# Kernel tuning notes

Hardware: AMD Instinct MI355X
Metric: run time of the kernel (lower is better)

The kernel has to match this reference:

```python
import jax, jax.numpy as jnp
import numpy as np

# Model config (matches init_kwargs)
B, T, D = 2, 2048, 2048
H, KH, F = 16, 4, 8192
HD = D // H            # 128
G = H // KH            # q heads per kv head = 4
EPS = 1e-5


def _ln(x, g, b):
    m = jnp.mean(x, axis=-1, keepdims=True)
    v = jnp.mean((x - m) ** 2, axis=-1, keepdims=True)
    return (x - m) * jax.lax.rsqrt(v + EPS) * g + b


def setup_inputs() -> dict:
    key = jax.random.key(0)
    ks = jax.random.split(key, 8)

    def xav(k, shape):
        lim = (6.0 / (shape[0] + shape[1])) ** 0.5
        return jax.random.uniform(k, shape, jnp.float32, -lim, lim)

    x = jax.random.normal(ks[0], (B, T, D), jnp.float32)
    mask = jnp.tril(jnp.ones((1, 1, T, T), jnp.int32))  # causal
    # Linear weights stored as [in, out] (transpose of torch nn.Linear)
    return {
        "x": x,
        "mask": mask,
        "Wq": xav(ks[1], (D, H * HD)), "bq": jnp.zeros((H * HD,), jnp.float32),
        "Wk": xav(ks[2], (D, KH * HD)), "bk": jnp.zeros((KH * HD,), jnp.float32),
        "Wv": xav(ks[3], (D, KH * HD)), "bv": jnp.zeros((KH * HD,), jnp.float32),
        "Wo": xav(ks[4], (H * HD, D)), "bo": jnp.zeros((D,), jnp.float32),
        "ln1_g": jnp.ones((D,), jnp.float32), "ln1_b": jnp.zeros((D,), jnp.float32),
        "ln2_g": jnp.ones((D,), jnp.float32), "ln2_b": jnp.zeros((D,), jnp.float32),
        "fln_g": jnp.ones((D,), jnp.float32), "fln_b": jnp.zeros((D,), jnp.float32),
        "W1": xav(ks[5], (D, F)), "b1": jnp.zeros((F,), jnp.float32),
        "W2": xav(ks[6], (D, F)), "b2": jnp.zeros((F,), jnp.float32),
        "W3": xav(ks[7], (F, D)), "b3": jnp.zeros((D,), jnp.float32),
    }


def reference(x, mask, Wq, bq, Wk, bk, Wv, bv, Wo, bo,
              ln1_g, ln1_b, ln2_g, ln2_b, fln_g, fln_b,
              W1, b1, W2, b2, W3, b3):
    scale = 1.0 / np.sqrt(HD)
    # --- attention block (pre-LN + residual) ---
    h = _ln(x, ln1_g, ln1_b)
    q = (h @ Wq + bq).reshape(B, T, KH, G, HD)   # q head k*G+g uses kv head k
    k = (h @ Wk + bk).reshape(B, T, KH, HD)
    v = (h @ Wv + bv).reshape(B, T, KH, HD)
    # GQA scores without repeat_interleave: broadcast kv head across group g
    scores = jnp.einsum('btkgd,bskd->bkgts', q, k) * scale  # [B,KH,G,T,T]
    scores = jnp.clip(scores, -100.0, 100.0)
    scores = jnp.where(mask[:, :, None] == 0, -jnp.inf, scores)
    attn = jax.nn.softmax(scores, axis=-1)
    ctx = jnp.einsum('bkgts,bskd->btkgd', attn, v).reshape(B, T, H * HD)
    x = x + (ctx @ Wo + bo)  # dropout is identity in eval
    # --- ln2 then SwiGLU FFN (which has its own internal LN and residual
    # around the *post-ln2* activation, faithful to original) ---
    x = _ln(x, ln2_g, ln2_b)
    r = x
    h2 = _ln(x, fln_g, fln_b)
    g_pre = h2 @ W1 + b1
    gate = g_pre * jax.nn.sigmoid(jnp.clip(g_pre, -10.0, 10.0))
    hidden = h2 @ W2 + b2
    return r + ((gate * hidden) @ W3 + b3)
```

## Files before the change

kernel.cpp:

```cpp
#include <hip/hip_runtime.h>
#include <math.h>
#include <stdint.h>

typedef __bf16 bf16_t;
typedef __bf16 bf16x4 __attribute__((ext_vector_type(4)));
typedef __bf16 bf16x8 __attribute__((ext_vector_type(8)));
typedef float  f32x4  __attribute__((ext_vector_type(4)));

#define D_MODEL 2048
#define T_SEQ   2048
#define BATCH   2
#define NROWS   (BATCH*T_SEQ)
#define NHEAD   16
#define HDIM    128
#define KVH     4
#define KVD     (KVH*HDIM)
#define FDIM    8192
#define QKVN    3072

__device__ __forceinline__ bf16x8 mk8(bf16x4 lo, bf16x4 hi) {
  union { bf16x4 h[2]; bf16x8 v; } u;
  u.h[0] = lo; u.h[1] = hi; return u.v;
}

__device__ __forceinline__ void gl16(const bf16_t* g, bf16_t* l) {
  __builtin_amdgcn_global_load_lds(
      (const uint32_t __attribute__((address_space(1)))*)g,
      (uint32_t __attribute__((address_space(3)))*)l, 16, 0, 0);
}

__global__ __launch_bounds__(256)
void transpose_w(const float* __restrict__ in, bf16_t* __restrict__ outT, int K, int N)
{
  __shared__ __align__(16) bf16_t t[64][72];
  const int tid = threadIdx.x;
  const int k0 = blockIdx.y * 64, n0 = blockIdx.x * 64;
  const int tr = tid >> 4, tc = (tid & 15) * 4;
#pragma unroll
  for (int i = 0; i < 4; ++i) {
    f32x4 v = *(const f32x4*)(in + (size_t)(k0 + tr + 16 * i) * N + n0 + tc);
#pragma unroll
    for (int e = 0; e < 4; ++e) t[tr + 16 * i][tc + e] = (bf16_t)v[e];
  }
  __syncthreads();
#pragma unroll
  for (int s = 0; s < 2; ++s) {
    const int c = s * 256 + tid;
    const int n = c >> 3, c8 = (c & 7) * 8;
    bf16x8 o;
#pragma unroll
    for (int e = 0; e < 8; ++e) o[e] = t[c8 + e][n];
    *(bf16x8*)(outT + (size_t)(n0 + n) * K + k0 + c8) = o;
  }
}

__global__ __launch_bounds__(256)
void concat_bias(const float* __restrict__ a, const float* __restrict__ b,
                 const float* __restrict__ c, float* __restrict__ dst)
{
  const int i = blockIdx.x * 256 + threadIdx.x;
  if (i >= QKVN) return;
  dst[i] = (i < 2048) ? a[i] : (i < 2560) ? b[i - 2048] : c[i - 2560];
}

template<typename TI>
__global__ __launch_bounds__(256)
void ln_kernel(const TI* __restrict__ x, const float* __restrict__ g,
               const float* __restrict__ b, bf16_t* __restrict__ out)
{
  const int row = blockIdx.x;
  const int tid = threadIdx.x;
  const TI* xr = x + (size_t)row * D_MODEL;
  float vals[8];
  if constexpr (sizeof(TI) == 4) {
    f32x4 v0 = *(const f32x4*)(xr + tid * 8);
    f32x4 v1 = *(const f32x4*)(xr + tid * 8 + 4);
#pragma unroll
    for (int e = 0; e < 4; ++e) { vals[e] = v0[e]; vals[4 + e] = v1[e]; }
  } else {
    bf16x8 v = *(const bf16x8*)(xr + tid * 8);
#pragma unroll
    for (int e = 0; e < 8; ++e) vals[e] = (float)v[e];
  }
  float s = 0.f, s2 = 0.f;
#pragma unroll
  for (int e = 0; e < 8; ++e) { s += vals[e]; s2 += vals[e] * vals[e]; }
#pragma unroll
  for (int off = 1; off < 64; off <<= 1) { s += __shfl_xor(s, off); s2 += __shfl_xor(s2, off); }
  __shared__ float red[8];
  const int wid = tid >> 6, lane = tid & 63;
  if (lane == 0) { red[wid] = s; red[4 + wid] = s2; }
  __syncthreads();
  s  = red[0] + red[1] + red[2] + red[3];
  s2 = red[4] + red[5] + red[6] + red[7];
  const float mean = s * (1.f / D_MODEL);
  const float var  = s2 * (1.f / D_MODEL) - mean * mean;
  const float rstd = rsqrtf(var + 1e-5f);
  f32x4 g0 = *(const f32x4*)(g + tid * 8), g1 = *(const f32x4*)(g + tid * 8 + 4);
  f32x4 b0 = *(const f32x4*)(b + tid * 8), b1 = *(const f32x4*)(b + tid * 8 + 4);
  bf16x8 o;
#pragma unroll
  for (int e = 0; e < 4; ++e) {
    o[e]     = (bf16_t)((vals[e]     - mean) * rstd * g0[e] + b0[e]);
    o[4 + e] = (bf16_t)((vals[4 + e] - mean) * rstd * g1[e] + b1[e]);
  }
  *(bf16x8*)(out + (size_t)row * D_MODEL + tid * 8) = o;
}

__global__ __launch_bounds__(256)
void ln2_fused(const bf16_t* __restrict__ x, const float* __restrict__ g2,
               const float* __restrict__ b2, const float* __restrict__ gf,
               const float* __restrict__ bf_, bf16_t* __restrict__ rout,
               bf16_t* __restrict__ hout)
{
  const int row = blockIdx.x;
  const int tid = threadIdx.x;
  const int wid = tid >> 6, lane = tid & 63;
  __shared__ float red[8];
  const bf16_t* xr = x + (size_t)row * D_MODEL;
  bf16x8 v = *(const bf16x8*)(xr + tid * 8);
  float vals[8]; float s = 0.f, s2 = 0.f;
#pragma unroll
  for (int e = 0; e < 8; ++e) { vals[e] = (float)v[e]; s += vals[e]; s2 += vals[e] * vals[e]; }
#pragma unroll
  for (int off = 1; off < 64; off <<= 1) { s += __shfl_xor(s, off); s2 += __shfl_xor(s2, off); }
  if (lane == 0) { red[wid] = s; red[4 + wid] = s2; }
  __syncthreads();
  s  = red[0] + red[1] + red[2] + red[3];
  s2 = red[4] + red[5] + red[6] + red[7];
  float mean = s * (1.f / D_MODEL);
  float var  = s2 * (1.f / D_MODEL) - mean * mean;
  float rstd = rsqrtf(var + 1e-5f);
  f32x4 ga0 = *(const f32x4*)(g2 + tid * 8), ga1 = *(const f32x4*)(g2 + tid * 8 + 4);
  f32x4 ba0 = *(const f32x4*)(b2 + tid * 8), ba1 = *(const f32x4*)(b2 + tid * 8 + 4);
  float y[8];
#pragma unroll
  for (int e = 0; e < 4; ++e) {
    y[e]     = (vals[e]     - mean) * rstd * ga0[e] + ba0[e];
    y[4 + e] = (vals[4 + e] - mean) * rstd * ga1[e] + ba1[e];
  }
  bf16x8 o1;
#pragma unroll
  for (int e = 0; e < 8; ++e) o1[e] = (bf16_t)y[e];
  *(bf16x8*)(rout + (size_t)row * D_MODEL + tid * 8) = o1;
  s = 0.f; s2 = 0.f;
#pragma unroll
  for (int e = 0; e < 8; ++e) { s += y[e]; s2 += y[e] * y[e]; }
#pragma unroll
  for (int off = 1; off < 64; off <<= 1) { s += __shfl_xor(s, off); s2 += __shfl_xor(s2, off); }
  __syncthreads();
  if (lane == 0) { red[wid] = s; red[4 + wid] = s2; }
  __syncthreads();
  s  = red[0] + red[1] + red[2] + red[3];
  s2 = red[4] + red[5] + red[6] + red[7];
  mean = s * (1.f / D_MODEL);
  var  = s2 * (1.f / D_MODEL) - mean * mean;
  rstd = rsqrtf(var + 1e-5f);
  f32x4 gb0 = *(const f32x4*)(gf + tid * 8), gb1 = *(const f32x4*)(gf + tid * 8 + 4);
  f32x4 bb0 = *(const f32x4*)(bf_ + tid * 8), bb1 = *(const f32x4*)(bf_ + tid * 8 + 4);
  bf16x8 o2;
#pragma unroll
  for (int e = 0; e < 4; ++e) {
    o2[e]     = (bf16_t)((y[e]     - mean) * rstd * gb0[e] + bb0[e]);
    o2[4 + e] = (bf16_t)((y[4 + e] - mean) * rstd * gb1[e] + bb1[e]);
  }
  *(bf16x8*)(hout + (size_t)row * D_MODEL + tid * 8) = o2;
}

enum { EPI_NONE = 0, EPI_RES = 1, EPI_SILU = 2, EPI_MUL = 3 };

__device__ __forceinline__ void xcd_swz(int BMv, int BNv, int& m0, int& n0) {
  const int nbx = gridDim.x, nwg = nbx * gridDim.y;
  int flat = blockIdx.y * nbx + blockIdx.x;
  flat = (flat & 7) * (nwg >> 3) + (flat >> 3);
  m0 = (flat / nbx) * BMv; n0 = (flat % nbx) * BNv;
}

template<int EPI, int BM_T, typename TE, typename TO>
__global__ __launch_bounds__(512, 2)
void gemm8p(const bf16_t* __restrict__ A, const bf16_t* __restrict__ Bt,
            const float* __restrict__ bias, const TE* __restrict__ extra,
            TO* __restrict__ out, int M, int N, int K)
{
  constexpr int ALs = BM_T / 128;
  constexpr int RF  = BM_T / 32;
  __shared__ __align__(16) bf16_t As[2][2][BM_T * 32];
  __shared__ __align__(16) bf16_t Bs[2][2][256 * 32];
  const int tid = threadIdx.x, lane = tid & 63, wid = tid >> 6;
  const int wr = wid >> 2, wc = wid & 3;
  const int l16 = lane & 15, lq = lane >> 4;
  int m0, n0; xcd_swz(BM_T, 256, m0, n0);

  const bf16_t* aP[ALs]; int aL[ALs];
#pragma unroll
  for (int s = 0; s < ALs; ++s) {
    const int c = s * 512 + tid;
    const int row = c >> 2, pos = c & 3;
    aP[s] = A + (size_t)(m0 + row) * K + (pos ^ ((row >> 1) & 3)) * 8;
    aL[s] = (s * 512 + wid * 64) * 8;
  }
  const bf16_t* bP[2]; int bL[2];
#pragma unroll
  for (int s = 0; s < 2; ++s) {
    const int c = s * 512 + tid;
    const int row = c >> 2, pos = c & 3;
    bP[s] = Bt + (size_t)(n0 + row) * K + (pos ^ ((row >> 1) & 3)) * 8;
    bL[s] = (s * 512 + wid * 64) * 8;
  }

  int offA[RF];
#pragma unroll
  for (int i = 0; i < RF; ++i) {
    const int r = wr * (BM_T / 2) + i * 16 + l16;
    offA[i] = r * 32 + ((lq ^ ((r >> 1) & 3)) * 8);
  }
  int offB[4];
#pragma unroll
  for (int jj = 0; jj < 4; ++jj) {
    const int r = wc * 64 + jj * 16 + l16;
    offB[jj] = r * 32 + ((lq ^ ((r >> 1) & 3)) * 8);
  }

  f32x4 acc[RF][4];
#pragma unroll
  for (int i = 0; i < RF; ++i)
#pragma unroll
    for (int j = 0; j < 4; ++j) acc[i][j] = (f32x4){0.f, 0.f, 0.f, 0.f};

  auto SA = [&](int t, int bb, int kh) {
#pragma unroll
    for (int s = 0; s < ALs; ++s) gl16(aP[s] + t * 64 + kh * 32, &As[bb][kh][aL[s]]);
  };
  auto SB = [&](int t, int bb, int kh) {
#pragma unroll
    for (int s = 0; s < 2; ++s) gl16(bP[s] + t * 64 + kh * 32, &Bs[bb][kh][bL[s]]);
  };
#define BAR_()  __builtin_amdgcn_s_barrier()
#define LGKM_() do { asm volatile("s_waitcnt lgkmcnt(0)" ::: "memory"); \
                     __builtin_amdgcn_sched_barrier(0); } while (0)

  const int nt = K >> 6;
  SA(0, 0, 0); SB(0, 0, 0); SA(0, 0, 1); SB(0, 0, 1);
  if (nt > 1) { SA(1, 1, 0); SB(1, 1, 0); SA(1, 1, 1); }
  if (nt > 2) {
    if constexpr (ALs == 2) asm volatile("s_waitcnt vmcnt(6)" ::: "memory");
    else                    asm volatile("s_waitcnt vmcnt(4)" ::: "memory");
  } else {
    asm volatile("s_waitcnt vmcnt(0)" ::: "memory");
  }
  BAR_();

  for (int t = 0; t < nt; ++t) {
    const int b = t & 1, ob = b ^ 1;
    const bool s1 = (t + 1 < nt), s2 = (t + 2 < nt);
    bf16x8 af[RF], bf0, bf1;
    if (s1) SB(t + 1, ob, 1);
#pragma unroll
    for (int i = 0; i < RF; ++i) af[i] = *(const bf16x8*)(&As[b][0][offA[i]]);
    bf0 = *(const bf16x8*)(&Bs[b][0][offB[0]]);
    bf1 = *(const bf16x8*)(&Bs[b][0][offB[1]]);
    BAR_(); LGKM_();
    __builtin_amdgcn_s_setprio(1);
#pragma unroll
    for (int i = 0; i < RF; ++i) {
      acc[i][0] = __builtin_amdgcn_mfma_f32_16x16x32_bf16(af[i], bf0, acc[i][0], 0, 0, 0);
      acc[i][1] = __builtin_amdgcn_mfma_f32_16x16x32_bf16(af[i], bf1, acc[i][1], 0, 0, 0);
    }
    __builtin_amdgcn_s_setprio(0);
    BAR_();
    if (s2) SA(t + 2, b, 0);
    bf0 = *(const bf16x8*)(&Bs[b][0][offB[2]]);
    bf1 = *(const bf16x8*)(&Bs[b][0][offB[3]]);
    BAR_(); LGKM_();
    __builtin_amdgcn_s_setprio(1);
#pragma unroll
    for (int i = 0; i < RF; ++i) {
      acc[i][2] = __builtin_amdgcn_mfma_f32_16x16x32_bf16(af[i], bf0, acc[i][2], 0, 0, 0);
      acc[i][3] = __builtin_amdgcn_mfma_f32_16x16x32_bf16(af[i], bf1, acc[i][3], 0, 0, 0);
    }
    __builtin_amdgcn_s_setprio(0);
    BAR_();
    if (s2) SB(t + 2, b, 0);
#pragma unroll
    for (int i = 0; i < RF; ++i) af[i] = *(const bf16x8*)(&As[b][1][offA[i]]);
    bf0 = *(const bf16x8*)(&Bs[b][1][offB[0]]);
    bf1 = *(const bf16x8*)(&Bs[b][1][offB[1]]);
    BAR_(); LGKM_();
    __builtin_amdgcn_s_setprio(1);
#pragma unroll
    for (int i = 0; i < RF; ++i) {
      acc[i][0] = __builtin_amdgcn_mfma_f32_16x16x32_bf16(af[i], bf0, acc[i][0], 0, 0, 0);
      acc[i][1] = __builtin_amdgcn_mfma_f32_16x16x32_bf16(af[i], bf1, acc[i][1], 0, 0, 0);
    }
    __builtin_amdgcn_s_setprio(0);
    BAR_();
    if (s2) SA(t + 2, b, 1);
    bf0 = *(const bf16x8*)(&Bs[b][1][offB[2]]);
    bf1 = *(const bf16x8*)(&Bs[b][1][offB[3]]);
    BAR_(); LGKM_();
    __builtin_amdgcn_s_setprio(1);
#pragma unroll
    for (int i = 0; i < RF; ++i) {
      acc[i][2] = __builtin_amdgcn_mfma_f32_16x16x32_bf16(af[i], bf0, acc[i][2], 0, 0, 0);
      acc[i][3] = __builtin_amdgcn_mfma_f32_16x16x32_bf16(af[i], bf1, acc[i][3], 0, 0, 0);
    }
    __builtin_amdgcn_s_setprio(0);
    if (t < nt - 2) {
      if constexpr (ALs == 2) asm volatile("s_waitcnt vmcnt(6)" ::: "memory");
      else                    asm volatile("s_waitcnt vmcnt(4)" ::: "memory");
    } else {
      asm volatile("s_waitcnt vmcnt(0)" ::: "memory");
    }
    BAR_();
  }

  if constexpr (sizeof(TO) == 2) {
    bf16_t* sc = &As[0][0][0] + (size_t)wid * (16 * 72);
    const int rr = lane >> 3, cc8 = (lane & 7) * 8;
#pragma unroll
    for (int i = 0; i < RF; ++i) {
      const int row0 = m0 + wr * (BM_T / 2) + i * 16;
#pragma unroll
      for (int j = 0; j < 4; ++j) {
        const int col = n0 + wc * 64 + j * 16 + l16;
        const float bb = bias[col];
#pragma unroll
        for (int e = 0; e < 4; ++e) {
          const size_t idx = (size_t)(row0 + lq * 4 + e) * N + col;
          float vv = acc[i][j][e] + bb;
          if (EPI == EPI_RES)       vv += (float)extra[idx];
          else if (EPI == EPI_SILU) { float c2 = fminf(fmaxf(vv, -10.f), 10.f); vv = vv / (1.f + __expf(-c2)); }
          else if (EPI == EPI_MUL)  vv *= (float)extra[idx];
          sc[(lq * 4 + e) * 72 + j * 16 + l16] = (bf16_t)vv;
        }
      }
      asm volatile("s_waitcnt lgkmcnt(0)" ::: "memory");
      __builtin_amdgcn_sched_barrier(0);
#pragma unroll
      for (int q = 0; q < 2; ++q) {
        bf16x8 v8 = *(const bf16x8*)(sc + (rr + q * 8) * 72 + cc8);
        *(bf16x8*)(out + (size_t)(row0 + rr + q * 8) * N + n0 + wc * 64 + cc8) = v8;
      }
      asm volatile("s_waitcnt lgkmcnt(0)" ::: "memory");
      __builtin_amdgcn_sched_barrier(0);
    }
  } else {
#pragma unroll
    for (int j = 0; j < 4; ++j) {
      const int col = n0 + wc * 64 + j * 16 + l16;
      const float bb = bias[col];
#pragma unroll
      for (int i = 0; i < RF; ++i) {
        const int row0 = m0 + wr * (BM_T / 2) + i * 16 + lq * 4;
#pragma unroll
        for (int e = 0; e < 4; ++e) {
          const size_t idx = (size_t)(row0 + e) * N + col;
          float vv = acc[i][j][e] + bb;
          if (EPI == EPI_RES)       vv += (float)extra[idx];
          else if (EPI == EPI_SILU) { float c2 = fminf(fmaxf(vv, -10.f), 10.f); vv = vv / (1.f + __expf(-c2)); }
          else if (EPI == EPI_MUL)  vv *= (float)extra[idx];
          out[idx] = (TO)vv;
        }
      }
    }
  }
#undef BAR_
#undef LGKM_
}

template<int EPI, typename TE, typename TO>
__global__ __launch_bounds__(512, 2)
void gemm2p(const bf16_t* __restrict__ A, const bf16_t* __restrict__ Bt,
            const float* __restrict__ bias, const TE* __restrict__ extra,
            TO* __restrict__ out, int M, int N, int K)
{
  __shared__ __align__(16) bf16_t As[2][2][128 * 32];
  __shared__ __align__(16) bf16_t Bs[2][2][256 * 32];
  const int tid = threadIdx.x, lane = tid & 63, wid = tid >> 6;
  const int wr = wid >> 2, wc = wid & 3;
  const int l16 = lane & 15, lq = lane >> 4;
  int m0, n0; xcd_swz(128, 256, m0, n0);

  const bf16_t* aP; int aL;
  {
    const int row = tid >> 2, pos = tid & 3;
    aP = A + (size_t)(m0 + row) * K + (pos ^ ((row >> 1) & 3)) * 8;
    aL = (wid * 64) * 8;
  }
  const bf16_t* bP[2]; int bL[2];
#pragma unroll
  for (int s = 0; s < 2; ++s) {
    const int c = s * 512 + tid;
    const int row = c >> 2, pos = c & 3;
    bP[s] = Bt + (size_t)(n0 + row) * K + (pos ^ ((row >> 1) & 3)) * 8;
    bL[s] = (s * 512 + wid * 64) * 8;
  }

  int offA[4], offB[4];
#pragma unroll
  for (int i = 0; i < 4; ++i) {
    const int r = wr * 64 + i * 16 + l16;
    offA[i] = r * 32 + ((lq ^ ((r >> 1) & 3)) * 8);
  }
#pragma unroll
  for (int j = 0; j < 4; ++j) {
    const int r = wc * 64 + j * 16 + l16;
    offB[j] = r * 32 + ((lq ^ ((r >> 1) & 3)) * 8);
  }

  f32x4 acc[4][4];
#pragma unroll
  for (int i = 0; i < 4; ++i)
#pragma unroll
    for (int j = 0; j < 4; ++j) acc[i][j] = (f32x4){0.f, 0.f, 0.f, 0.f};

  auto SA = [&](int t, int bb, int kh) { gl16(aP + t * 64 + kh * 32, &As[bb][kh][aL]); };
  auto SB = [&](int t, int bb, int kh) {
#pragma unroll
    for (int s = 0; s < 2; ++s) gl16(bP[s] + t * 64 + kh * 32, &Bs[bb][kh][bL[s]]);
  };

  const int nt = K >> 6;
  SA(0, 0, 0); SB(0, 0, 0); SA(0, 0, 1); SB(0, 0, 1);
  if (nt > 1) {
    SA(1, 1, 0); SB(1, 1, 0);
    asm volatile("s_waitcnt vmcnt(3)" ::: "memory");
  } else {
    asm volatile("s_waitcnt vmcnt(0)" ::: "memory");
  }
  __builtin_amdgcn_s_barrier();

  for (int t = 0; t < nt; ++t) {
    const int b = t & 1, ob = b ^ 1;
    bf16x8 af[4], bfr[4];
    if (t + 1 < nt) { SA(t + 1, ob, 1); SB(t + 1, ob, 1); }
#pragma unroll
    for (int i = 0; i < 4; ++i) af[i]  = *(const bf16x8*)(&As[b][0][offA[i]]);
#pragma unroll
    for (int j = 0; j < 4; ++j) bfr[j] = *(const bf16x8*)(&Bs[b][0][offB[j]]);
    __builtin_amdgcn_s_barrier();
    asm volatile("s_waitcnt lgkmcnt(0)" ::: "memory");
    __builtin_amdgcn_sched_barrier(0);
    __builtin_amdgcn_s_setprio(1);
#pragma unroll
    for (int i = 0; i < 4; ++i)
#pragma unroll
      for (int j = 0; j < 4; ++j)
        acc[i][j] = __builtin_amdgcn_mfma_f32_16x16x32_bf16(af[i], bfr[j], acc[i][j], 0, 0, 0);
    __builtin_amdgcn_s_setprio(0);
    __builtin_amdgcn_s_barrier();
    if (t + 2 < nt) { SA(t + 2, b, 0); SB(t + 2, b, 0); }
#pragma unroll
    for (int i = 0; i < 4; ++i) af[i]  = *(const bf16x8*)(&As[b][1][offA[i]]);
#pragma unroll
    for (int j = 0; j < 4; ++j) bfr[j] = *(const bf16x8*)(&Bs[b][1][offB[j]]);
    if (t + 2 < nt) asm volatile("s_waitcnt vmcnt(3)" ::: "memory");
    else            asm volatile("s_waitcnt vmcnt(0)" ::: "memory");
    __builtin_amdgcn_s_barrier();
    asm volatile("s_waitcnt lgkmcnt(0)" ::: "memory");
    __builtin_amdgcn_sched_barrier(0);
    __builtin_amdgcn_s_setprio(1);
#pragma unroll
    for (int i = 0; i < 4; ++i)
#pragma unroll
      for (int j = 0; j < 4; ++j)
        acc[i][j] = __builtin_amdgcn_mfma_f32_16x16x32_bf16(af[i], bfr[j], acc[i][j], 0, 0, 0);
    __builtin_amdgcn_s_setprio(0);
    __builtin_amdgcn_s_barrier();
  }

  if constexpr (sizeof(TO) == 2) {
    bf16_t* sc = &As[0][0][0] + (size_t)wid * (16 * 72);
    const int rr = lane >> 3, cc8 = (lane & 7) * 8;
#pragma unroll
    for (int i = 0; i < 4; ++i) {
      const int row0 = m0 + wr * 64 + i * 16;
#pragma unroll
      for (int j = 0; j < 4; ++j) {
        const int col = n0 + wc * 64 + j * 16 + l16;
        const float bb = bias[col];
#pragma unroll
        for (int e = 0; e < 4; ++e) {
          const size_t idx = (size_t)(row0 + lq * 4 + e) * N + col;
          float vv = acc[i][j][e] + bb;
          if (EPI == EPI_RES)       vv += (float)extra[idx];
          else if (EPI == EPI_SILU) { float c2 = fminf(fmaxf(vv, -10.f), 10.f); vv = vv / (1.f + __expf(-c2)); }
          else if (EPI == EPI_MUL)  vv *= (float)extra[idx];
          sc[(lq * 4 + e) * 72 + j * 16 + l16] = (bf16_t)vv;
        }
      }
      asm volatile("s_waitcnt lgkmcnt(0)" ::: "memory");
      __builtin_amdgcn_sched_barrier(0);
#pragma unroll
      for (int q = 0; q < 2; ++q) {
        bf16x8 v8 = *(const bf16x8*)(sc + (rr + q * 8) * 72 + cc8);
        *(bf16x8*)(out + (size_t)(row0 + rr + q * 8) * N + n0 + wc * 64 + cc8) = v8;
      }
      asm volatile("s_waitcnt lgkmcnt(0)" ::: "memory");
      __builtin_amdgcn_sched_barrier(0);
    }
  } else {
#pragma unroll
    for (int j = 0; j < 4; ++j) {
      const int col = n0 + wc * 64 + j * 16 + l16;
      const float bb = bias[col];
#pragma unroll
      for (int i = 0; i < 4; ++i) {
        const int row0 = m0 + wr * 64 + i * 16 + lq * 4;
#pragma unroll
        for (int e = 0; e < 4; ++e) {
          const size_t idx = (size_t)(row0 + e) * N + col;
          float vv = acc[i][j][e] + bb;
          if (EPI == EPI_RES)       vv += (float)extra[idx];
          else if (EPI == EPI_SILU) { float c2 = fminf(fmaxf(vv, -10.f), 10.f); vv = vv / (1.f + __expf(-c2)); }
          else if (EPI == EPI_MUL)  vv *= (float)extra[idx];
          out[idx] = (TO)vv;
        }
      }
    }
  }
}

template<int EPI, typename TE, typename TO>
__global__ __launch_bounds__(256)
void gemm_kernel(const bf16_t* __restrict__ A, const float* __restrict__ W,
                 const float* __restrict__ bias, const TE* __restrict__ extra,
                 TO* __restrict__ out, int M, int N, int K)
{
  __shared__ bf16_t As[128][40];
  __shared__ bf16_t Bs[128][40];
  const int tid  = threadIdx.x;
  const int lane = tid & 63, wid = tid >> 6;
  const int wr = wid >> 1, wc = wid & 1;
  const int l16 = lane & 15, lq = lane >> 4;
  const int m0 = blockIdx.y * 128, n0 = blockIdx.x * 128;

  f32x4 acc[4][4];
#pragma unroll
  for (int i = 0; i < 4; ++i)
#pragma unroll
    for (int j = 0; j < 4; ++j) acc[i][j] = (f32x4){0.f, 0.f, 0.f, 0.f};

  const int ar = tid >> 1, ah = tid & 1;
  const int kk = tid & 31, cc = tid >> 5;

  for (int k0 = 0; k0 < K; k0 += 32) {
    const bf16_t* asrc = A + (size_t)(m0 + ar) * K + k0 + ah * 16;
    *(bf16x8*)(&As[ar][ah * 16])     = *(const bf16x8*)(asrc);
    *(bf16x8*)(&As[ar][ah * 16 + 8]) = *(const bf16x8*)(asrc + 8);
    const float* wsrc = W + (size_t)(k0 + kk) * N + n0;
#pragma unroll
    for (int it = 0; it < 2; ++it) {
      const int c = cc * 8 + it * 64;
      f32x4 wa = *(const f32x4*)(wsrc + c);
      f32x4 wb = *(const f32x4*)(wsrc + c + 4);
#pragma unroll
      for (int e = 0; e < 4; ++e) {
        Bs[c + e][kk]     = (bf16_t)wa[e];
        Bs[c + 4 + e][kk] = (bf16_t)wb[e];
      }
    }
    __syncthreads();
    bf16x8 af[4], bfr[4];
#pragma unroll
    for (int i = 0; i < 4; ++i) {
      const bf16_t* p = &As[wr * 64 + i * 16 + l16][lq * 4];
      af[i] = mk8(*(const bf16x4*)p, *(const bf16x4*)(p + 16));
    }
#pragma unroll
    for (int j = 0; j < 4; ++j) {
      const bf16_t* p = &Bs[wc * 64 + j * 16 + l16][lq * 4];
      bfr[j] = mk8(*(const bf16x4*)p, *(const bf16x4*)(p + 16));
    }
#pragma unroll
    for (int i = 0; i < 4; ++i)
#pragma unroll
      for (int j = 0; j < 4; ++j)
        acc[i][j] = __builtin_amdgcn_mfma_f32_16x16x32_bf16(af[i], bfr[j], acc[i][j], 0, 0, 0);
    __syncthreads();
  }

#pragma unroll
  for (int j = 0; j < 4; ++j) {
    const int col = n0 + wc * 64 + j * 16 + l16;
    const float bb = bias[col];
#pragma unroll
    for (int i = 0; i < 4; ++i) {
      const int row0 = m0 + wr * 64 + i * 16 + lq * 4;
#pragma unroll
      for (int e = 0; e < 4; ++e) {
        const size_t idx = (size_t)(row0 + e) * N + col;
        float vv = acc[i][j][e] + bb;
        if (EPI == EPI_RES)       vv += (float)extra[idx];
        else if (EPI == EPI_SILU) { float c2 = fminf(fmaxf(vv, -10.f), 10.f); vv = vv / (1.f + __expf(-c2)); }
        else if (EPI == EPI_MUL)  vv *= (float)extra[idx];
        out[idx] = (TO)vv;
      }
    }
  }
}

__global__ __launch_bounds__(256)
void attn_kernel(const bf16_t* __restrict__ q, const bf16_t* __restrict__ k,
                 const bf16_t* __restrict__ v, bf16_t* __restrict__ ctx,
                 int q_ld, int kv_ld)
{
  __shared__ __align__(16) bf16_t Ks[64 * 128];
  __shared__ __align__(16) bf16_t Vt[128][72];

  const int tid = threadIdx.x, lane = tid & 63, wid = tid >> 6;
  const int l16 = lane & 15, lq = lane >> 4;
  const int bh = blockIdx.y;
  const int b = bh >> 4, h = bh & 15;
  const int kh = h >> 2;
  const float scale = 0.08838834764831845f;

  for (int pass = 0; pass < 2; ++pass) {
    const int qt = pass ? blockIdx.x : (31 - blockIdx.x);
    const int qbase = qt * 64;
    const int qrow = qbase + wid * 16 + l16;

    const bf16_t* qp = q + (size_t)(b * T_SEQ + qrow) * q_ld + h * HDIM;
    bf16x8 bq[4];
#pragma unroll
    for (int s = 0; s < 4; ++s) bq[s] = *(const bf16x8*)(qp + s * 32 + lq * 8);

    float m_r = -1e30f, l_r = 0.f;
    f32x4 acc_o[8];
#pragma unroll
    for (int jh = 0; jh < 8; ++jh) acc_o[jh] = (f32x4){0.f, 0.f, 0.f, 0.f};

    const int ntiles = qt + 1;
    for (int t = 0; t < ntiles; ++t) {
      const int kb = t * 64;
      __syncthreads();
#pragma unroll
      for (int it = 0; it < 4; ++it) {
        const int c = it * 256 + tid;
        const int kvr = c >> 4, pos = c & 15;
        const int src = pos ^ (kvr & 7);
        gl16(k + (size_t)(b * T_SEQ + kb + kvr) * kv_ld + kh * HDIM + src * 8,
             Ks + (size_t)(it * 256 + wid * 64) * 8);
      }
#pragma unroll
      for (int it = 0; it < 4; ++it) {
        const int c = tid + it * 256;
        const int r = c & 63, voff = (c >> 6) * 8;
        bf16x8 vv = *(const bf16x8*)(v + (size_t)(b * T_SEQ + kb + r) * kv_ld + kh * HDIM + voff);
#pragma unroll
        for (int e = 0; e < 8; ++e) Vt[voff + e][r] = vv[e];
      }
      __syncthreads();

      f32x4 sf[4];
#pragma unroll
      for (int j = 0; j < 4; ++j) {
        sf[j] = (f32x4){0.f, 0.f, 0.f, 0.f};
        const int kvr = j * 16 + l16;
#pragma unroll
        for (int s = 0; s < 4; ++s) {
          bf16x8 ak = *(const bf16x8*)(Ks + kvr * 128 + (((s * 4 + lq) ^ (kvr & 7)) * 8));
          sf[j] = __builtin_amdgcn_mfma_f32_16x16x32_bf16(ak, bq[s], sf[j], 0, 0, 0);
        }
      }

      float p[4][4];
      float tmax = -1e30f;
#pragma unroll
      for (int j = 0; j < 4; ++j)
#pragma unroll
        for (int e = 0; e < 4; ++e) {
          const int kvc = kb + j * 16 + lq * 4 + e;
          float sv = sf[j][e] * scale;
          sv = fminf(fmaxf(sv, -100.f), 100.f);
          if (kvc > qrow) sv = -1e30f;
          p[j][e] = sv;
          tmax = fmaxf(tmax, sv);
        }
      tmax = fmaxf(tmax, __shfl_xor(tmax, 16));
      tmax = fmaxf(tmax, __shfl_xor(tmax, 32));
      const float mnew = fmaxf(m_r, tmax);
      const float resc = __expf(m_r - mnew);
      m_r = mnew;
      float rsum = 0.f;
#pragma unroll
      for (int j = 0; j < 4; ++j)
#pragma unroll
        for (int e = 0; e < 4; ++e) {
          p[j][e] = __expf(p[j][e] - m_r);
          rsum += p[j][e];
        }
      rsum += __shfl_xor(rsum, 16);
      rsum += __shfl_xor(rsum, 32);
      l_r = l_r * resc + rsum;

      float resc4[4];
#pragma unroll
      for (int e = 0; e < 4; ++e) resc4[e] = __shfl(resc, lq * 4 + e);
#pragma unroll
      for (int jh = 0; jh < 8; ++jh)
#pragma unroll
        for (int e = 0; e < 4; ++e) acc_o[jh][e] *= resc4[e];

      bf16x8 pa[2];
#pragma unroll
      for (int sk = 0; sk < 2; ++sk) {
        bf16x4 lo, hi;
#pragma unroll
        for (int e = 0; e < 4; ++e) { lo[e] = (bf16_t)p[2 * sk][e]; hi[e] = (bf16_t)p[2 * sk + 1][e]; }
        pa[sk] = mk8(lo, hi);
      }
#pragma unroll
      for (int jh = 0; jh < 8; ++jh) {
#pragma unroll
        for (int sk = 0; sk < 2; ++sk) {
          const bf16_t* pV = &Vt[jh * 16 + l16][sk * 32 + lq * 4];
          bf16x8 bv2 = mk8(*(const bf16x4*)pV, *(const bf16x4*)(pV + 16));
          acc_o[jh] = __builtin_amdgcn_mfma_f32_16x16x32_bf16(pa[sk], bv2, acc_o[jh], 0, 0, 0);
        }
      }
    }

    float l4[4];
#pragma unroll
    for (int e = 0; e < 4; ++e) l4[e] = __shfl(l_r, lq * 4 + e);
    bf16_t* op = ctx + (size_t)(b * T_SEQ + qbase + wid * 16) * D_MODEL + h * HDIM;
#pragma unroll
    for (int jh = 0; jh < 8; ++jh)
#pragma unroll
      for (int e = 0; e < 4; ++e)
        op[(size_t)(lq * 4 + e) * D_MODEL + jh * 16 + l16] = (bf16_t)(acc_o[jh][e] / l4[e]);
  }
}

extern "C" void kernel_launch(void* const* d_in, const int* in_sizes, int n_in,
                              void* d_out, int out_size, void* d_ws, size_t ws_size,
                              hipStream_t stream)
{
  const float* x   = (const float*)d_in[0];
  const float* Wq  = (const float*)d_in[2];
  const float* bq  = (const float*)d_in[3];
  const float* Wk  = (const float*)d_in[4];
  const float* bk  = (const float*)d_in[5];
  const float* Wv  = (const float*)d_in[6];
  const float* bv  = (const float*)d_in[7];
  const float* Wo  = (const float*)d_in[8];
  const float* bo  = (const float*)d_in[9];
  const float* g1  = (const float*)d_in[10];
  const float* b1n = (const float*)d_in[11];
  const float* g2  = (const float*)d_in[12];
  const float* b2n = (const float*)d_in[13];
  const float* gf  = (const float*)d_in[14];
  const float* bfn = (const float*)d_in[15];
  const float* W1  = (const float*)d_in[16];
  const float* bb1 = (const float*)d_in[17];
  const float* W2  = (const float*)d_in[18];
  const float* bb2 = (const float*)d_in[19];
  const float* W3  = (const float*)d_in[20];
  const float* bb3 = (const float*)d_in[21];
  float* out = (float*)d_out;

  char* ws = (char*)d_ws;
  size_t off = 0;
  auto alloc = [&](size_t bytes) -> void* {
    void* p = ws + off; off += (bytes + 255) & ~(size_t)255; return p;
  };
  const dim3 blk(256);

  bf16_t* Wt_qkv = (bf16_t*)alloc((size_t)QKVN * D_MODEL * 2);
  bf16_t* Wt_o   = (bf16_t*)alloc((size_t)D_MODEL * D_MODEL * 2);
  bf16_t* Wt1    = (bf16_t*)alloc((size_t)FDIM * D_MODEL * 2);
  bf16_t* Wt2    = (bf16_t*)alloc((size_t)FDIM * D_MODEL * 2);
  bf16_t* Wt3    = (bf16_t*)alloc((size_t)D_MODEL * FDIM * 2);
  float*  bqkv   = (float*)alloc((size_t)QKVN * 4);
  bf16_t* hbuf   = (bf16_t*)alloc((size_t)NROWS * D_MODEL * 2);
  bf16_t* qkvbuf = (bf16_t*)alloc((size_t)NROWS * QKVN * 2);
  bf16_t* rbuf   = (bf16_t*)alloc((size_t)NROWS * D_MODEL * 2);
  bf16_t* h2buf  = (bf16_t*)alloc((size_t)NROWS * D_MODEL * 2);
  const size_t core = off;

  if (core <= ws_size) {
    size_t avail = ws_size - core;
    int chunk = (int)((avail / ((size_t)FDIM * 2)) & ~(size_t)255);
    bf16_t* gbuf;
    if (chunk >= 256) { gbuf = (bf16_t*)(ws + core); if (chunk > NROWS) chunk = NROWS; }
    else              { gbuf = qkvbuf; chunk = 1536; }
    bf16_t* x1buf = qkvbuf;

    transpose_w<<<dim3(32, 32),  blk, 0, stream>>>(Wq, Wt_qkv, D_MODEL, 2048);
    transpose_w<<<dim3(8, 32),   blk, 0, stream>>>(Wk, Wt_qkv + (size_t)2048 * D_MODEL, D_MODEL, 512);
    transpose_w<<<dim3(8, 32),   blk, 0, stream>>>(Wv, Wt_qkv + (size_t)2560 * D_MODEL, D_MODEL, 512);
    transpose_w<<<dim3(32, 32),  blk, 0, stream>>>(Wo, Wt_o, D_MODEL, D_MODEL);
    transpose_w<<<dim3(128, 32), blk, 0, stream>>>(W1, Wt1, D_MODEL, FDIM);
    transpose_w<<<dim3(128, 32), blk, 0, stream>>>(W2, Wt2, D_MODEL, FDIM);
    transpose_w<<<dim3(32, 128), blk, 0, stream>>>(W3, Wt3, FDIM, D_MODEL);
    concat_bias<<<12, blk, 0, stream>>>(bq, bk, bv, bqkv);

    ln_kernel<float><<<NROWS, blk, 0, stream>>>(x, g1, b1n, hbuf);
    gemm8p<EPI_NONE, 256, bf16_t, bf16_t><<<dim3(QKVN / 256, NROWS / 256), 512, 0, stream>>>(
        hbuf, Wt_qkv, bqkv, nullptr, qkvbuf, NROWS, QKVN, D_MODEL);
    attn_kernel<<<dim3(16, 32), blk, 0, stream>>>(
        qkvbuf, qkvbuf + 2048, qkvbuf + 2560, hbuf, QKVN, QKVN);
    gemm2p<EPI_RES, float, bf16_t><<<dim3(D_MODEL / 256, NROWS / 128), 512, 0, stream>>>(
        hbuf, Wt_o, bo, x, x1buf, NROWS, D_MODEL, D_MODEL);
    ln2_fused<<<NROWS, blk, 0, stream>>>(x1buf, g2, b2n, gf, bfn, rbuf, h2buf);

    for (int r0 = 0; r0 < NROWS; r0 += chunk) {
      const int rows = (NROWS - r0 < chunk) ? (NROWS - r0) : chunk;
      gemm8p<EPI_SILU, 256, bf16_t, bf16_t><<<dim3(FDIM / 256, rows / 256), 512, 0, stream>>>(
          h2buf + (size_t)r0 * D_MODEL, Wt1, bb1, nullptr, gbuf, rows, FDIM, D_MODEL);
      gemm8p<EPI_MUL, 256, bf16_t, bf16_t><<<dim3(FDIM / 256, rows / 256), 512, 0, stream>>>(
          h2buf + (size_t)r0 * D_MODEL, Wt2, bb2, gbuf, gbuf, rows, FDIM, D_MODEL);
      gemm2p<EPI_RES, bf16_t, float><<<dim3(D_MODEL / 256, rows / 128), 512, 0, stream>>>(
          gbuf, Wt3, bb3, rbuf + (size_t)r0 * D_MODEL, out + (size_t)r0 * D_MODEL, rows, D_MODEL, FDIM);
    }
    return;
  }

  off = 0;
  const size_t DBYTES = (size_t)NROWS * D_MODEL * 2;
  bf16_t* fhbuf  = (bf16_t*)alloc(DBYTES);
  bf16_t* fqbuf  = (bf16_t*)alloc(DBYTES);
  bf16_t* fkbuf  = (bf16_t*)alloc((size_t)NROWS * KVD * 2);
  bf16_t* fvbuf  = (bf16_t*)alloc((size_t)NROWS * KVD * 2);
  bf16_t* frbuf  = (bf16_t*)alloc(DBYTES);
  bf16_t* fh2buf = (bf16_t*)alloc(DBYTES);
  const size_t base = off;
  size_t avail = (ws_size > base) ? (ws_size - base) : 0;
  int chunk = (int)((avail / ((size_t)FDIM * 2)) & ~(size_t)127);
  bf16_t* gbuf;
  if (chunk >= 128) { gbuf = (bf16_t*)(ws + base); if (chunk > NROWS) chunk = NROWS; }
  else              { gbuf = fqbuf; chunk = 1024; }

  ln_kernel<float><<<NROWS, blk, 0, stream>>>(x, g1, b1n, fhbuf);
  gemm_kernel<EPI_NONE, bf16_t, bf16_t><<<dim3(16, 32), blk, 0, stream>>>(fhbuf, Wq, bq, nullptr, fqbuf, NROWS, 2048, 2048);
  gemm_kernel<EPI_NONE, bf16_t, bf16_t><<<dim3(4, 32),  blk, 0, stream>>>(fhbuf, Wk, bk, nullptr, fkbuf, NROWS, 512, 2048);
  gemm_kernel<EPI_NONE, bf16_t, bf16_t><<<dim3(4, 32),  blk, 0, stream>>>(fhbuf, Wv, bv, nullptr, fvbuf, NROWS, 512, 2048);
  attn_kernel<<<dim3(16, 32), blk, 0, stream>>>(fqbuf, fkbuf, fvbuf, fhbuf, 2048, 512);
  gemm_kernel<EPI_RES, float, bf16_t><<<dim3(16, 32), blk, 0, stream>>>(fhbuf, Wo, bo, x, fqbuf, NROWS, 2048, 2048);
  ln_kernel<bf16_t><<<NROWS, blk, 0, stream>>>(fqbuf, g2, b2n, frbuf);
  ln_kernel<bf16_t><<<NROWS, blk, 0, stream>>>(frbuf, gf, bfn, fh2buf);
  for (int r0 = 0; r0 < NROWS; r0 += chunk) {
    const int rows = (NROWS - r0 < chunk) ? (NROWS - r0) : chunk;
    gemm_kernel<EPI_SILU, bf16_t, bf16_t><<<dim3(64, rows / 128), blk, 0, stream>>>(
        fh2buf + (size_t)r0 * D_MODEL, W1, bb1, nullptr, gbuf, rows, FDIM, 2048);
    gemm_kernel<EPI_MUL, bf16_t, bf16_t><<<dim3(64, rows / 128), blk, 0, stream>>>(
        fh2buf + (size_t)r0 * D_MODEL, W2, bb2, gbuf, gbuf, rows, FDIM, 2048);
    gemm_kernel<EPI_RES, bf16_t, float><<<dim3(16, rows / 128), blk, 0, stream>>>(
        gbuf, W3, bb3, frbuf + (size_t)r0 * D_MODEL, out + (size_t)r0 * D_MODEL, rows, 2048, FDIM);
  }
}
```

Baseline: 906.3 us.

## Replace 128x256 two-phase GEMM with 128x128 triple-buffered GEMM for N=2048 projections

Adds a new 256-thread GEMM kernel with 128x128 tiles, K-step 32 and a three-stage LDS ring buffer, and uses it for the output projection and the W3 down-projection in place of the 512-thread 128x256 kernel. The smaller tiles double the number of workgroups for the N=2048 GEMMs, so the GPU's compute units should be better filled and the tail wave shrinks, at the cost of lower per-block operand reuse. The 8-wave GEMM also reorders its global-to-LDS prefetch issue to come after the LDS fragment reads in each phase. That reordering changes when loads are queued relative to the LDS reads.

```diff
diff --git a/kernel.cpp b/kernel.cpp
--- a/kernel.cpp
+++ b/kernel.cpp
@@ -174,6 +174,141 @@
   int flat = blockIdx.y * nbx + blockIdx.x;
   flat = (flat & 7) * (nwg >> 3) + (flat >> 3);
   m0 = (flat / nbx) * BMv; n0 = (flat % nbx) * BNv;
+}
+
+template<int EPI, typename TE, typename TO>
+__global__ __launch_bounds__(256, 4)
+void gemm3b(const bf16_t* __restrict__ A, const bf16_t* __restrict__ Bt,
+            const float* __restrict__ bias, const TE* __restrict__ extra,
+            TO* __restrict__ out, int M, int N, int K)
+{
+  __shared__ __align__(16) bf16_t As[3][128 * 32];
+  __shared__ __align__(16) bf16_t Bs[3][128 * 32];
+  const int tid = threadIdx.x, lane = tid & 63, wid = tid >> 6;
+  const int wr = wid >> 1, wc = wid & 1;
+  const int l16 = lane & 15, lq = lane >> 4;
+  int m0, n0; xcd_swz(128, 128, m0, n0);
+
+  const bf16_t* aP[2]; const bf16_t* bP[2]; int sL[2];
+#pragma unroll
+  for (int s = 0; s < 2; ++s) {
+    const int c = s * 256 + tid;
+    const int row = c >> 2, pos = c & 3;
+    const int g = pos ^ ((row >> 1) & 3);
+    aP[s] = A  + (size_t)(m0 + row) * K + g * 8;
+    bP[s] = Bt + (size_t)(n0 + row) * K + g * 8;
+    sL[s] = (s * 256 + wid * 64) * 8;
+  }
+
+  int offA[4], offB[4];
+#pragma unroll
+  for (int i = 0; i < 4; ++i) {
+    const int r = wr * 64 + i * 16 + l16;
+    offA[i] = r * 32 + ((lq ^ ((r >> 1) & 3)) * 8);
+  }
+#pragma unroll
+  for (int j = 0; j < 4; ++j) {
+    const int r = wc * 64 + j * 16 + l16;
+    offB[j] = r * 32 + ((lq ^ ((r >> 1) & 3)) * 8);
+  }
+
+  f32x4 acc[4][4];
+#pragma unroll
+  for (int i = 0; i < 4; ++i)
+#pragma unroll
+    for (int j = 0; j < 4; ++j) acc[i][j] = (f32x4){0.f, 0.f, 0.f, 0.f};
+
+  auto STAGE = [&](int t, int b) {
+    gl16(aP[0] + t * 32, &As[b][sL[0]]);
+    gl16(aP[1] + t * 32, &As[b][sL[1]]);
+    gl16(bP[0] + t * 32, &Bs[b][sL[0]]);
+    gl16(bP[1] + t * 32, &Bs[b][sL[1]]);
+  };
+
+  const int nt = K >> 5;
+  STAGE(0, 0);
+  STAGE(1, 1);
+  if (nt > 1) asm volatile("s_waitcnt vmcnt(4)" ::: "memory");
+  else        asm volatile("s_waitcnt vmcnt(0)" ::: "memory");
+  __builtin_amdgcn_s_barrier();
+
+  int b = 0;
+  for (int t = 0; t < nt; ++t) {
+    bf16x8 af[4], bfr[4];
+#pragma unroll
+    for (int i = 0; i < 4; ++i) af[i]  = *(const bf16x8*)(&As[b][offA[i]]);
+#pragma unroll
+    for (int j = 0; j < 4; ++j) bfr[j] = *(const bf16x8*)(&Bs[b][offB[j]]);
+    if (t + 2 < nt) {
+      STAGE(t + 2, (b + 2) % 3);
+      asm volatile("s_waitcnt vmcnt(4)" ::: "memory");
+    } else {
+      asm volatile("s_waitcnt vmcnt(0)" ::: "memory");
+    }
+    __builtin_amdgcn_s_barrier();
+    asm volatile("s_waitcnt lgkmcnt(0)" ::: "memory");
+    __builtin_amdgcn_sched_barrier(0);
+    __builtin_amdgcn_s_setprio(1);
+#pragma unroll
+    for (int i = 0; i < 4; ++i)
+#pragma unroll
+      for (int j = 0; j < 4; ++j)
+        acc[i][j] = __builtin_amdgcn_mfma_f32_16x16x32_bf16(af[i], bfr[j], acc[i][j], 0, 0, 0);
+    __builtin_amdgcn_s_setprio(0);
+    __builtin_amdgcn_s_barrier();
+    b = (b + 1) % 3;
+  }
+
+  if constexpr (sizeof(TO) == 2) {
+    bf16_t* sc = &As[0][0] + (size_t)wid * (16 * 72);
+    const int rr = lane >> 3, cc8 = (lane & 7) * 8;
+#pragma unroll
+    for (int i = 0; i < 4; ++i) {
+      const int row0 = m0 + wr * 64 + i * 16;
+#pragma unroll
+      for (int j = 0; j < 4; ++j) {
+        const int col = n0 + wc * 64 + j * 16 + l16;
+        const float bb = bias[col];
+#pragma unroll
+        for (int e = 0; e < 4; ++e) {
+          const size_t idx = (size_t)(row0 + lq * 4 + e) * N + col;
+          float vv = acc[i][j][e] + bb;
+          if (EPI == EPI_RES)       vv += (float)extra[idx];
+          else if (EPI == EPI_SILU) { float c2 = fminf(fmaxf(vv, -10.f), 10.f); vv = vv / (1.f + __expf(-c2)); }
+          else if (EPI == EPI_MUL)  vv *= (float)extra[idx];
+          sc[(lq * 4 + e) * 72 + j * 16 + l16] = (bf16_t)vv;
+        }
+      }
+      asm volatile("s_waitcnt lgkmcnt(0)" ::: "memory");
+      __builtin_amdgcn_sched_barrier(0);
+#pragma unroll
+      for (int q = 0; q < 2; ++q) {
+        bf16x8 v8 = *(const bf16x8*)(sc + (rr + q * 8) * 72 + cc8);
+        *(bf16x8*)(out + (size_t)(row0 + rr + q * 8) * N + n0 + wc * 64 + cc8) = v8;
+      }
+      asm volatile("s_waitcnt lgkmcnt(0)" ::: "memory");
+      __builtin_amdgcn_sched_barrier(0);
+    }
+  } else {
+#pragma unroll
+    for (int j = 0; j < 4; ++j) {
+      const int col = n0 + wc * 64 + j * 16 + l16;
+      const float bb = bias[col];
+#pragma unroll
+      for (int i = 0; i < 4; ++i) {
+        const int row0 = m0 + wr * 64 + i * 16 + lq * 4;
+#pragma unroll
+        for (int e = 0; e < 4; ++e) {
+          const size_t idx = (size_t)(row0 + e) * N + col;
+          float vv = acc[i][j][e] + bb;
+          if (EPI == EPI_RES)       vv += (float)extra[idx];
+          else if (EPI == EPI_SILU) { float c2 = fminf(fmaxf(vv, -10.f), 10.f); vv = vv / (1.f + __expf(-c2)); }
+          else if (EPI == EPI_MUL)  vv *= (float)extra[idx];
+          out[idx] = (TO)vv;
+        }
+      }
+    }
+  }
 }
 
 template<int EPI, int BM_T, typename TE, typename TO>
@@ -254,11 +389,11 @@
     const int b = t & 1, ob = b ^ 1;
     const bool s1 = (t + 1 < nt), s2 = (t + 2 < nt);
     bf16x8 af[RF], bf0, bf1;
-    if (s1) SB(t + 1, ob, 1);
 #pragma unroll
     for (int i = 0; i < RF; ++i) af[i] = *(const bf16x8*)(&As[b][0][offA[i]]);
     bf0 = *(const bf16x8*)(&Bs[b][0][offB[0]]);
     bf1 = *(const bf16x8*)(&Bs[b][0][offB[1]]);
+    if (s1) SB(t + 1, ob, 1);
     BAR_(); LGKM_();
     __builtin_amdgcn_s_setprio(1);
 #pragma unroll
@@ -268,9 +403,9 @@
     }
     __builtin_amdgcn_s_setprio(0);
     BAR_();
-    if (s2) SA(t + 2, b, 0);
     bf0 = *(const bf16x8*)(&Bs[b][0][offB[2]]);
     bf1 = *(const bf16x8*)(&Bs[b][0][offB[3]]);
+    if (s2) SA(t + 2, b, 0);
     BAR_(); LGKM_();
     __builtin_amdgcn_s_setprio(1);
 #pragma unroll
@@ -280,11 +415,11 @@
     }
     __builtin_amdgcn_s_setprio(0);
     BAR_();
-    if (s2) SB(t + 2, b, 0);
 #pragma unroll
     for (int i = 0; i < RF; ++i) af[i] = *(const bf16x8*)(&As[b][1][offA[i]]);
     bf0 = *(const bf16x8*)(&Bs[b][1][offB[0]]);
     bf1 = *(const bf16x8*)(&Bs[b][1][offB[1]]);
+    if (s2) SB(t + 2, b, 0);
     BAR_(); LGKM_();
     __builtin_amdgcn_s_setprio(1);
 #pragma unroll
@@ -294,9 +429,9 @@
     }
     __builtin_amdgcn_s_setprio(0);
     BAR_();
-    if (s2) SA(t + 2, b, 1);
     bf0 = *(const bf16x8*)(&Bs[b][1][offB[2]]);
     bf1 = *(const bf16x8*)(&Bs[b][1][offB[3]]);
+    if (s2) SA(t + 2, b, 1);
     BAR_(); LGKM_();
     __builtin_amdgcn_s_setprio(1);
 #pragma unroll
@@ -366,159 +501,6 @@
   }
 #undef BAR_
 #undef LGKM_
-}
-
-template<int EPI, typename TE, typename TO>
-__global__ __launch_bounds__(512, 2)
-void gemm2p(const bf16_t* __restrict__ A, const bf16_t* __restrict__ Bt,
-            const float* __restrict__ bias, const TE* __restrict__ extra,
-            TO* __restrict__ out, int M, int N, int K)
-{
-  __shared__ __align__(16) bf16_t As[2][2][128 * 32];
-  __shared__ __align__(16) bf16_t Bs[2][2][256 * 32];
-  const int tid = threadIdx.x, lane = tid & 63, wid = tid >> 6;
-  const int wr = wid >> 2, wc = wid & 3;
-  const int l16 = lane & 15, lq = lane >> 4;
-  int m0, n0; xcd_swz(128, 256, m0, n0);
-
-  const bf16_t* aP; int aL;
-  {
-    const int row = tid >> 2, pos = tid & 3;
-    aP = A + (size_t)(m0 + row) * K + (pos ^ ((row >> 1) & 3)) * 8;
-    aL = (wid * 64) * 8;
-  }
-  const bf16_t* bP[2]; int bL[2];
-#pragma unroll
-  for (int s = 0; s < 2; ++s) {
-    const int c = s * 512 + tid;
-    const int row = c >> 2, pos = c & 3;
-    bP[s] = Bt + (size_t)(n0 + row) * K + (pos ^ ((row >> 1) & 3)) * 8;
-    bL[s] = (s * 512 + wid * 64) * 8;
-  }
-
-  int offA[4], offB[4];
-#pragma unroll
-  for (int i = 0; i < 4; ++i) {
-    const int r = wr * 64 + i * 16 + l16;
-    offA[i] = r * 32 + ((lq ^ ((r >> 1) & 3)) * 8);
-  }
-#pragma unroll
-  for (int j = 0; j < 4; ++j) {
-    const int r = wc * 64 + j * 16 + l16;
-    offB[j] = r * 32 + ((lq ^ ((r >> 1) & 3)) * 8);
-  }
-
-  f32x4 acc[4][4];
-#pragma unroll
-  for (int i = 0; i < 4; ++i)
-#pragma unroll
-    for (int j = 0; j < 4; ++j) acc[i][j] = (f32x4){0.f, 0.f, 0.f, 0.f};
-
-  auto SA = [&](int t, int bb, int kh) { gl16(aP + t * 64 + kh * 32, &As[bb][kh][aL]); };
-  auto SB = [&](int t, int bb, int kh) {
-#pragma unroll
-    for (int s = 0; s < 2; ++s) gl16(bP[s] + t * 64 + kh * 32, &Bs[bb][kh][bL[s]]);
-  };
-
-  const int nt = K >> 6;
-  SA(0, 0, 0); SB(0, 0, 0); SA(0, 0, 1); SB(0, 0, 1);
-  if (nt > 1) {
-    SA(1, 1, 0); SB(1, 1, 0);
-    asm volatile("s_waitcnt vmcnt(3)" ::: "memory");
-  } else {
-    asm volatile("s_waitcnt vmcnt(0)" ::: "memory");
-  }
-  __builtin_amdgcn_s_barrier();
-
-  for (int t = 0; t < nt; ++t) {
-    const int b = t & 1, ob = b ^ 1;
-    bf16x8 af[4], bfr[4];
-    if (t + 1 < nt) { SA(t + 1, ob, 1); SB(t + 1, ob, 1); }
-#pragma unroll
-    for (int i = 0; i < 4; ++i) af[i]  = *(const bf16x8*)(&As[b][0][offA[i]]);
-#pragma unroll
-    for (int j = 0; j < 4; ++j) bfr[j] = *(const bf16x8*)(&Bs[b][0][offB[j]]);
-    __builtin_amdgcn_s_barrier();
-    asm volatile("s_waitcnt lgkmcnt(0)" ::: "memory");
-    __builtin_amdgcn_sched_barrier(0);
-    __builtin_amdgcn_s_setprio(1);
-#pragma unroll
-    for (int i = 0; i < 4; ++i)
-#pragma unroll
-      for (int j = 0; j < 4; ++j)
-        acc[i][j] = __builtin_amdgcn_mfma_f32_16x16x32_bf16(af[i], bfr[j], acc[i][j], 0, 0, 0);
-    __builtin_amdgcn_s_setprio(0);
-    __builtin_amdgcn_s_barrier();
-    if (t + 2 < nt) { SA(t + 2, b, 0); SB(t + 2, b, 0); }
-#pragma unroll
-    for (int i = 0; i < 4; ++i) af[i]  = *(const bf16x8*)(&As[b][1][offA[i]]);
-#pragma unroll
-    for (int j = 0; j < 4; ++j) bfr[j] = *(const bf16x8*)(&Bs[b][1][offB[j]]);
-    if (t + 2 < nt) asm volatile("s_waitcnt vmcnt(3)" ::: "memory");
-    else            asm volatile("s_waitcnt vmcnt(0)" ::: "memory");
-    __builtin_amdgcn_s_barrier();
-    asm volatile("s_waitcnt lgkmcnt(0)" ::: "memory");
-    __builtin_amdgcn_sched_barrier(0);
-    __builtin_amdgcn_s_setprio(1);
-#pragma unroll
-    for (int i = 0; i < 4; ++i)
-#pragma unroll
-      for (int j = 0; j < 4; ++j)
-        acc[i][j] = __builtin_amdgcn_mfma_f32_16x16x32_bf16(af[i], bfr[j], acc[i][j], 0, 0, 0);
-    __builtin_amdgcn_s_setprio(0);
-    __builtin_amdgcn_s_barrier();
-  }
-
-  if constexpr (sizeof(TO) == 2) {
-    bf16_t* sc = &As[0][0][0] + (size_t)wid * (16 * 72);
-    const int rr = lane >> 3, cc8 = (lane & 7) * 8;
-#pragma unroll
-    for (int i = 0; i < 4; ++i) {
-      const int row0 = m0 + wr * 64 + i * 16;
-#pragma unroll
-      for (int j = 0; j < 4; ++j) {
-        const int col = n0 + wc * 64 + j * 16 + l16;
-        const float bb = bias[col];
-#pragma unroll
-        for (int e = 0; e < 4; ++e) {
-          const size_t idx = (size_t)(row0 + lq * 4 + e) * N + col;
-          float vv = acc[i][j][e] + bb;
-          if (EPI == EPI_RES)       vv += (float)extra[idx];
-          else if (EPI == EPI_SILU) { float c2 = fminf(fmaxf(vv, -10.f), 10.f); vv = vv / (1.f + __expf(-c2)); }
-          else if (EPI == EPI_MUL)  vv *= (float)extra[idx];
-          sc[(lq * 4 + e) * 72 + j * 16 + l16] = (bf16_t)vv;
-        }
-      }
-      asm volatile("s_waitcnt lgkmcnt(0)" ::: "memory");
-      __builtin_amdgcn_sched_barrier(0);
-#pragma unroll
-      for (int q = 0; q < 2; ++q) {
-        bf16x8 v8 = *(const bf16x8*)(sc + (rr + q * 8) * 72 + cc8);
-        *(bf16x8*)(out + (size_t)(row0 + rr + q * 8) * N + n0 + wc * 64 + cc8) = v8;
-      }
-      asm volatile("s_waitcnt lgkmcnt(0)" ::: "memory");
-      __builtin_amdgcn_sched_barrier(0);
-    }
-  } else {
-#pragma unroll
-    for (int j = 0; j < 4; ++j) {
-      const int col = n0 + wc * 64 + j * 16 + l16;
-      const float bb = bias[col];
-#pragma unroll
-      for (int i = 0; i < 4; ++i) {
-        const int row0 = m0 + wr * 64 + i * 16 + lq * 4;
-#pragma unroll
-        for (int e = 0; e < 4; ++e) {
-          const size_t idx = (size_t)(row0 + e) * N + col;
-          float vv = acc[i][j][e] + bb;
-          if (EPI == EPI_RES)       vv += (float)extra[idx];
-          else if (EPI == EPI_SILU) { float c2 = fminf(fmaxf(vv, -10.f), 10.f); vv = vv / (1.f + __expf(-c2)); }
-          else if (EPI == EPI_MUL)  vv *= (float)extra[idx];
-          out[idx] = (TO)vv;
-        }
-      }
-    }
-  }
 }
 
 template<int EPI, typename TE, typename TO>
@@ -801,7 +783,7 @@
         hbuf, Wt_qkv, bqkv, nullptr, qkvbuf, NROWS, QKVN, D_MODEL);
     attn_kernel<<<dim3(16, 32), blk, 0, stream>>>(
         qkvbuf, qkvbuf + 2048, qkvbuf + 2560, hbuf, QKVN, QKVN);
-    gemm2p<EPI_RES, float, bf16_t><<<dim3(D_MODEL / 256, NROWS / 128), 512, 0, stream>>>(
+    gemm3b<EPI_RES, float, bf16_t><<<dim3(D_MODEL / 128, NROWS / 128), blk, 0, stream>>>(
         hbuf, Wt_o, bo, x, x1buf, NROWS, D_MODEL, D_MODEL);
     ln2_fused<<<NROWS, blk, 0, stream>>>(x1buf, g2, b2n, gf, bfn, rbuf, h2buf);
 
@@ -811,7 +793,7 @@
           h2buf + (size_t)r0 * D_MODEL, Wt1, bb1, nullptr, gbuf, rows, FDIM, D_MODEL);
       gemm8p<EPI_MUL, 256, bf16_t, bf16_t><<<dim3(FDIM / 256, rows / 256), 512, 0, stream>>>(
           h2buf + (size_t)r0 * D_MODEL, Wt2, bb2, gbuf, gbuf, rows, FDIM, D_MODEL);
-      gemm2p<EPI_RES, bf16_t, float><<<dim3(D_MODEL / 256, rows / 128), 512, 0, stream>>>(
+      gemm3b<EPI_RES, bf16_t, float><<<dim3(D_MODEL / 128, rows / 128), blk, 0, stream>>>(
           gbuf, Wt3, bb3, rbuf + (size_t)r0 * D_MODEL, out + (size_t)r0 * D_MODEL, rows, D_MODEL, FDIM);
     }
     return;
```

Measured after the change: 776.1 us. -14.4%, faster.
